# Kernel tuning notes

Measured on AMD Instinct MI355X. Metric: run time of the kernel, lower is better.

The kernel has to match this reference:

```python
import jax, jax.numpy as jnp
import numpy as np

N_NODES = 50000
N_EDGES = 800000
D_FEAT = 128


def setup_inputs() -> dict:
    key = jax.random.key(0)
    k1, k2, k3, k4 = jax.random.split(key, 4)
    x = jax.random.normal(k1, (N_NODES, D_FEAT), dtype=jnp.float32)
    vals = jax.random.uniform(k2, (N_EDGES,), dtype=jnp.float32)
    rows = jnp.sort(jax.random.randint(k3, (N_EDGES,), 0, N_NODES, dtype=jnp.int32))
    cols = jax.random.randint(k4, (N_EDGES,), 0, N_NODES, dtype=jnp.int32)
    return {"x": x, "vals": vals, "rows": rows, "cols": cols}


def reference(x, vals, rows, cols):
    # out = A @ x where A is sparse COO: out[r] += vals[e] * x[cols[e]] for each edge e with rows[e]==r
    messages = vals[:, None] * x[cols]  # [E, d]
    out = jax.ops.segment_sum(messages, rows, num_segments=N_NODES)  # [N, d]
    return out
```

## Files before the change

### kernel.cpp

```cpp
#include <hip/hip_runtime.h>


#define D_FEAT 128
#define EPW 128
#define WAVES_PER_BLOCK 4
#define BLOCK_THREADS 256
#define PF 8

typedef float v2f __attribute__((ext_vector_type(2)));

__device__ __forceinline__ float bcast_f(float v, int j) {
    return __int_as_float(__builtin_amdgcn_readlane(__float_as_int(v), j));
}

__device__ __forceinline__ unsigned short f2bf_rne(float f) {
    unsigned int b = __float_as_uint(f);
    b += 0x7fffu + ((b >> 16) & 1u);
    return (unsigned short)(b >> 16);
}

__global__ __launch_bounds__(256) void prep_kernel(
    const float* __restrict__ x, const float* __restrict__ vals,
    const int* __restrict__ cols, unsigned short* __restrict__ xb,
    unsigned int* __restrict__ cv, int n4, int n_edges) {
    const int tid = blockIdx.x * blockDim.x + threadIdx.x;
    const int nth = gridDim.x * blockDim.x;
    const float4* __restrict__ x4 = (const float4*)x;
    ushort4* __restrict__ o4 = (ushort4*)xb;
    for (int i = tid; i < n4; i += nth) {
        float4 f = x4[i];
        ushort4 o;
        o.x = f2bf_rne(f.x);
        o.y = f2bf_rne(f.y);
        o.z = f2bf_rne(f.z);
        o.w = f2bf_rne(f.w);
        o4[i] = o;
    }
    for (int e = tid; e < n_edges; e += nth) {
        cv[e] = ((unsigned int)cols[e] << 16) | (unsigned int)f2bf_rne(vals[e]);
    }
}

__global__ __launch_bounds__(BLOCK_THREADS) void agg_bf16_kernel(
    const unsigned int* __restrict__ xb,
    const unsigned int* __restrict__ cv,
    const int* __restrict__ rows, float* __restrict__ out, int n_edges) {
    const int wave = blockIdx.x * WAVES_PER_BLOCK + (threadIdx.x >> 6);
    const int lane = threadIdx.x & 63;

    const int start = wave * EPW;
    if (start >= n_edges) return;
    const int end = min(start + EPW, n_edges);

    const int first_row = rows[start];
    float2 acc = make_float2(0.f, 0.f);
    int cur_row = first_row;

    for (int e0 = start; e0 < end; e0 += 64) {
        const unsigned int mycv = __builtin_nontemporal_load(cv + e0 + lane);
        const int myr = __builtin_nontemporal_load(rows + e0 + lane);
        const int nxt = __shfl(myr, (lane + 1) & 63);
        const unsigned long long bmask =
            __ballot(myr != nxt) & 0x7fffffffffffffffULL;
        const int g0 = __builtin_amdgcn_readfirstlane(myr);
        if (g0 != cur_row) {
            float* o = out + (size_t)cur_row * D_FEAT + 2 * lane;
            if (cur_row == first_row) {
                atomicAdd(o, acc.x);
                atomicAdd(o + 1, acc.y);
            } else {
                v2f st; st.x = acc.x; st.y = acc.y;
                __builtin_nontemporal_store(st, (v2f*)o);
            }
            acc.x = 0.f; acc.y = 0.f;
            cur_row = g0;
        }
#pragma unroll
        for (int j0 = 0; j0 < 64; j0 += PF) {
            unsigned int sv[PF];
            unsigned int xu[PF];
#pragma unroll
            for (int t = 0; t < PF; ++t) {
                sv[t] = (unsigned int)__builtin_amdgcn_readlane((int)mycv, j0 + t);
                xu[t] = xb[(size_t)(sv[t] >> 16) * (D_FEAT / 2) + lane];
            }
#pragma unroll
            for (int t = 0; t < PF; ++t) {
                const float vf = __uint_as_float(sv[t] << 16);
                acc.x = fmaf(vf, __uint_as_float(xu[t] << 16), acc.x);
                acc.y = fmaf(vf, __uint_as_float(xu[t] & 0xffff0000u), acc.y);
                if ((bmask >> (j0 + t)) & 1ULL) {
                    const int fr = __builtin_amdgcn_readlane(myr, j0 + t);
                    float* o = out + (size_t)fr * D_FEAT + 2 * lane;
                    if (fr == first_row) {
                        atomicAdd(o, acc.x);
                        atomicAdd(o + 1, acc.y);
                    } else {
                        v2f st; st.x = acc.x; st.y = acc.y;
                        __builtin_nontemporal_store(st, (v2f*)o);
                    }
                    acc.x = 0.f; acc.y = 0.f;
                }
            }
        }
        cur_row = __builtin_amdgcn_readlane(myr, 63);
    }
    float* o = out + (size_t)cur_row * D_FEAT + 2 * lane;
    atomicAdd(o, acc.x);
    atomicAdd(o + 1, acc.y);
}

__global__ __launch_bounds__(BLOCK_THREADS) void agg_f32_kernel(
    const float* __restrict__ x, const float* __restrict__ vals,
    const int* __restrict__ rows, const int* __restrict__ cols,
    float* __restrict__ out, int n_edges, int epw) {
    const int wave = blockIdx.x * WAVES_PER_BLOCK + (threadIdx.x >> 6);
    const int lane = threadIdx.x & 63;

    const int start = wave * epw;
    if (start >= n_edges) return;
    int end = start + epw;
    if (end > n_edges) end = n_edges;

    const float2* __restrict__ x2 = (const float2*)x;
    const int first_row = rows[start];
    const int last_row  = rows[end - 1];

    float2 acc = make_float2(0.f, 0.f);
    int cur_row = first_row;

    for (int e0 = start; e0 < end; e0 += 64) {
        const int nb = min(end - e0, 64);
        int myc = 0, myr = 0;
        float myv = 0.f;
        if (lane < nb) {
            myc = cols[e0 + lane];
            myr = rows[e0 + lane];
            myv = vals[e0 + lane];
        }
        for (int j0 = 0; j0 < nb; j0 += PF) {
            const int m = min(nb - j0, PF);
            float2 xv[PF];
            int    rj[PF];
            float  vj[PF];
#pragma unroll
            for (int t = 0; t < PF; ++t) {
                if (t < m) {
                    const int cj = __builtin_amdgcn_readlane(myc, j0 + t);
                    rj[t] = __builtin_amdgcn_readlane(myr, j0 + t);
                    vj[t] = bcast_f(myv, j0 + t);
                    xv[t] = x2[(size_t)cj * (D_FEAT / 2) + lane];
                }
            }
#pragma unroll
            for (int t = 0; t < PF; ++t) {
                if (t < m) {
                    if (rj[t] != cur_row) {
                        float* o = out + (size_t)cur_row * D_FEAT + 2 * lane;
                        if (cur_row == first_row || cur_row == last_row) {
                            atomicAdd(o,     acc.x);
                            atomicAdd(o + 1, acc.y);
                        } else {
                            v2f st; st.x = acc.x; st.y = acc.y;
                            __builtin_nontemporal_store(st, (v2f*)o);
                        }
                        acc.x = 0.f; acc.y = 0.f;
                        cur_row = rj[t];
                    }
                    acc.x = fmaf(vj[t], xv[t].x, acc.x);
                    acc.y = fmaf(vj[t], xv[t].y, acc.y);
                }
            }
        }
    }
    float* o = out + (size_t)cur_row * D_FEAT + 2 * lane;
    atomicAdd(o,     acc.x);
    atomicAdd(o + 1, acc.y);
}

extern "C" void kernel_launch(void* const* d_in, const int* in_sizes, int n_in,
                              void* d_out, int out_size, void* d_ws, size_t ws_size,
                              hipStream_t stream) {
    const float* x    = (const float*)d_in[0];
    const float* vals = (const float*)d_in[1];
    const int*   rows = (const int*)d_in[2];
    const int*   cols = (const int*)d_in[3];
    float*       out  = (float*)d_out;

    const int n_edges = in_sizes[1];
    const int n_x     = in_sizes[0];
    const int n_nodes = out_size / D_FEAT;

    (void)hipMemsetAsync(d_out, 0, (size_t)out_size * sizeof(float), stream);

    const size_t xb_bytes = (size_t)n_x * sizeof(unsigned short);
    const size_t cv_off   = (xb_bytes + 255) & ~(size_t)255;
    const size_t need     = cv_off + (size_t)n_edges * sizeof(unsigned int);

    const bool fast_ok = (ws_size >= need) && (n_edges % 64 == 0) &&
                         (n_nodes <= 65536) && (n_x % 4 == 0);

    if (fast_ok) {
        unsigned short* xb = (unsigned short*)d_ws;
        unsigned int*   cv = (unsigned int*)((char*)d_ws + cv_off);
        prep_kernel<<<2048, 256, 0, stream>>>(x, vals, cols, xb, cv,
                                              n_x / 4, n_edges);
        const int waves  = (n_edges + EPW - 1) / EPW;
        const int blocks = (waves + WAVES_PER_BLOCK - 1) / WAVES_PER_BLOCK;
        agg_bf16_kernel<<<blocks, BLOCK_THREADS, 0, stream>>>(
            (const unsigned int*)xb, cv, rows, out, n_edges);
    } else {
        const int total_waves = 8192;
        const int epw    = (n_edges + total_waves - 1) / total_waves;
        const int blocks = total_waves / WAVES_PER_BLOCK;
        agg_f32_kernel<<<blocks, BLOCK_THREADS, 0, stream>>>(
            x, vals, rows, cols, out, n_edges, epw);
    }
}
```

Before: 119.7 us.

## Fuse memset, bf16 prep and aggregation into one cooperative kernel with grid sync

```diff
diff --git a/kernel.cpp b/kernel.cpp
--- a/kernel.cpp
+++ b/kernel.cpp
@@ -1,10 +1,14 @@
 #include <hip/hip_runtime.h>
+#include <hip/hip_cooperative_groups.h>
+
+namespace cg = cooperative_groups;
 
 
 #define D_FEAT 128
 #define EPW 128
 #define WAVES_PER_BLOCK 4
 #define BLOCK_THREADS 256
+#define COOP_BLOCKS 1024
 #define PF 8
 
 typedef float v2f __attribute__((ext_vector_type(2)));
@@ -17,6 +21,107 @@
     unsigned int b = __float_as_uint(f);
     b += 0x7fffu + ((b >> 16) & 1u);
     return (unsigned short)(b >> 16);
+}
+
+__global__ __launch_bounds__(BLOCK_THREADS) void fused_kernel(
+    const float* __restrict__ x, const float* __restrict__ vals,
+    const int* __restrict__ rows, const int* __restrict__ cols,
+    unsigned short* __restrict__ xb, unsigned int* __restrict__ cv,
+    float* __restrict__ out, int n4, int n_edges, int n_out4) {
+    const int tid = blockIdx.x * BLOCK_THREADS + threadIdx.x;
+    const int nth = gridDim.x * BLOCK_THREADS;
+
+    {
+        float4 z = make_float4(0.f, 0.f, 0.f, 0.f);
+        float4* __restrict__ oz = (float4*)out;
+        for (int i = tid; i < n_out4; i += nth) oz[i] = z;
+
+        const float4* __restrict__ x4 = (const float4*)x;
+        ushort4* __restrict__ xo = (ushort4*)xb;
+        for (int i = tid; i < n4; i += nth) {
+            float4 f = x4[i];
+            ushort4 o;
+            o.x = f2bf_rne(f.x);
+            o.y = f2bf_rne(f.y);
+            o.z = f2bf_rne(f.z);
+            o.w = f2bf_rne(f.w);
+            xo[i] = o;
+        }
+        for (int e = tid; e < n_edges; e += nth)
+            cv[e] = ((unsigned int)cols[e] << 16) | (unsigned int)f2bf_rne(vals[e]);
+    }
+
+    cg::this_grid().sync();
+
+    const unsigned int* __restrict__ xbu = (const unsigned int*)xb;
+    const int wave = blockIdx.x * WAVES_PER_BLOCK + (threadIdx.x >> 6);
+    const int lane = threadIdx.x & 63;
+
+    const int n_g = n_edges >> 6;
+    const int n_w = gridDim.x * WAVES_PER_BLOCK;
+    const int gb = n_g / n_w, gr = n_g % n_w;
+    const int myn = gb + (wave < gr ? 1 : 0);
+    if (myn == 0) return;
+    const int gfirst = wave * gb + min(wave, gr);
+    const int start = gfirst << 6;
+    const int end = (gfirst + myn) << 6;
+
+    const int first_row = rows[start];
+    float2 acc = make_float2(0.f, 0.f);
+    int cur_row = first_row;
+
+    for (int e0 = start; e0 < end; e0 += 64) {
+        const unsigned int mycv = __builtin_nontemporal_load(cv + e0 + lane);
+        const int myr = __builtin_nontemporal_load(rows + e0 + lane);
+        const int nxt = __shfl(myr, (lane + 1) & 63);
+        const unsigned long long bmask =
+            __ballot(myr != nxt) & 0x7fffffffffffffffULL;
+        const int grow0 = __builtin_amdgcn_readfirstlane(myr);
+        if (grow0 != cur_row) {
+            float* o = out + (size_t)cur_row * D_FEAT + 2 * lane;
+            if (cur_row == first_row) {
+                atomicAdd(o, acc.x);
+                atomicAdd(o + 1, acc.y);
+            } else {
+                v2f st; st.x = acc.x; st.y = acc.y;
+                __builtin_nontemporal_store(st, (v2f*)o);
+            }
+            acc.x = 0.f; acc.y = 0.f;
+            cur_row = grow0;
+        }
+#pragma unroll
+        for (int j0 = 0; j0 < 64; j0 += PF) {
+            unsigned int sv[PF];
+            unsigned int xu[PF];
+#pragma unroll
+            for (int t = 0; t < PF; ++t) {
+                sv[t] = (unsigned int)__builtin_amdgcn_readlane((int)mycv, j0 + t);
+                xu[t] = xbu[(size_t)(sv[t] >> 16) * (D_FEAT / 2) + lane];
+            }
+#pragma unroll
+            for (int t = 0; t < PF; ++t) {
+                const float vf = __uint_as_float(sv[t] << 16);
+                acc.x = fmaf(vf, __uint_as_float(xu[t] << 16), acc.x);
+                acc.y = fmaf(vf, __uint_as_float(xu[t] & 0xffff0000u), acc.y);
+                if ((bmask >> (j0 + t)) & 1ULL) {
+                    const int fr = __builtin_amdgcn_readlane(myr, j0 + t);
+                    float* o = out + (size_t)fr * D_FEAT + 2 * lane;
+                    if (fr == first_row) {
+                        atomicAdd(o, acc.x);
+                        atomicAdd(o + 1, acc.y);
+                    } else {
+                        v2f st; st.x = acc.x; st.y = acc.y;
+                        __builtin_nontemporal_store(st, (v2f*)o);
+                    }
+                    acc.x = 0.f; acc.y = 0.f;
+                }
+            }
+        }
+        cur_row = __builtin_amdgcn_readlane(myr, 63);
+    }
+    float* o = out + (size_t)cur_row * D_FEAT + 2 * lane;
+    atomicAdd(o, acc.x);
+    atomicAdd(o + 1, acc.y);
 }
 
 __global__ __launch_bounds__(256) void prep_kernel(
@@ -42,8 +147,7 @@
 }
 
 __global__ __launch_bounds__(BLOCK_THREADS) void agg_bf16_kernel(
-    const unsigned int* __restrict__ xb,
-    const unsigned int* __restrict__ cv,
+    const unsigned int* __restrict__ xb, const unsigned int* __restrict__ cv,
     const int* __restrict__ rows, float* __restrict__ out, int n_edges) {
     const int wave = blockIdx.x * WAVES_PER_BLOCK + (threadIdx.x >> 6);
     const int lane = threadIdx.x & 63;
@@ -191,29 +295,39 @@
     const int n_x     = in_sizes[0];
     const int n_nodes = out_size / D_FEAT;
 
-    (void)hipMemsetAsync(d_out, 0, (size_t)out_size * sizeof(float), stream);
-
     const size_t xb_bytes = (size_t)n_x * sizeof(unsigned short);
     const size_t cv_off   = (xb_bytes + 255) & ~(size_t)255;
     const size_t need     = cv_off + (size_t)n_edges * sizeof(unsigned int);
 
     const bool fast_ok = (ws_size >= need) && (n_edges % 64 == 0) &&
-                         (n_nodes <= 65536) && (n_x % 4 == 0);
+                         (n_nodes <= 65536) && (n_x % 4 == 0) &&
+                         (out_size % 4 == 0);
 
     if (fast_ok) {
         unsigned short* xb = (unsigned short*)d_ws;
         unsigned int*   cv = (unsigned int*)((char*)d_ws + cv_off);
+        int n4 = n_x / 4, ne = n_edges, n_out4 = out_size / 4;
+        void* args[] = {(void*)&x,  (void*)&vals, (void*)&rows, (void*)&cols,
+                        (void*)&xb, (void*)&cv,   (void*)&out,
+                        (void*)&n4, (void*)&ne,   (void*)&n_out4};
+        hipError_t err = hipLaunchCooperativeKernel(
+            fused_kernel, dim3(COOP_BLOCKS), dim3(BLOCK_THREADS), args, 0,
+            stream);
+        if (err == hipSuccess) return;
+        (void)hipMemsetAsync(d_out, 0, (size_t)out_size * sizeof(float), stream);
         prep_kernel<<<2048, 256, 0, stream>>>(x, vals, cols, xb, cv,
-                                              n_x / 4, n_edges);
+                                              n4, n_edges);
         const int waves  = (n_edges + EPW - 1) / EPW;
         const int blocks = (waves + WAVES_PER_BLOCK - 1) / WAVES_PER_BLOCK;
         agg_bf16_kernel<<<blocks, BLOCK_THREADS, 0, stream>>>(
             (const unsigned int*)xb, cv, rows, out, n_edges);
-    } else {
-        const int total_waves = 8192;
-        const int epw    = (n_edges + total_waves - 1) / total_waves;
-        const int blocks = total_waves / WAVES_PER_BLOCK;
-        agg_f32_kernel<<<blocks, BLOCK_THREADS, 0, stream>>>(
-            x, vals, rows, cols, out, n_edges, epw);
-    }
-}
+        return;
+    }
+
+    (void)hipMemsetAsync(d_out, 0, (size_t)out_size * sizeof(float), stream);
+    const int total_waves = 8192;
+    const int epw    = (n_edges + total_waves - 1) / total_waves;
+    const int blocks = total_waves / WAVES_PER_BLOCK;
+    agg_f32_kernel<<<blocks, BLOCK_THREADS, 0, stream>>>(
+        x, vals, rows, cols, out, n_edges, epw);
+}
```

After: 251.3 us. 2.1x slower.
